# Kernel optimization log

Measured on AMD Instinct MI355X. Metric: run time of the kernel, lower is better.

The kernel has to match this reference:

```python
import jax, jax.numpy as jnp
import numpy as np

B = 65536
IN_DIM = 512
H0, H1 = 256, 128
HEAD_H = 64
D = 12
K_MAX = 3
EPS = 1e-5
# predecessor indices per disease (topologically ordered DAG)
PRED_LISTS = [[], [0], [0], [1, 2], [0, 3], [2], [4, 5], [1, 6], [3, 7], [6, 8], [5, 9], [8, 10, 9]]


def setup_inputs() -> dict:
    key = jax.random.key(0)
    ks = jax.random.split(key, 16)
    x = jax.random.normal(ks[0], (B, IN_DIM), jnp.float32)
    enc_W0 = jax.random.normal(ks[1], (IN_DIM, H0), jnp.float32) * 0.04
    enc_b0 = jnp.zeros((H0,), jnp.float32)
    bn0_g = jnp.ones((H0,), jnp.float32)
    bn0_b = jnp.zeros((H0,), jnp.float32)
    bn0_m = jax.random.normal(ks[2], (H0,), jnp.float32) * 0.1
    bn0_v = jax.random.uniform(ks[3], (H0,), jnp.float32, 0.5, 1.5)
    enc_W1 = jax.random.normal(ks[4], (H0, H1), jnp.float32) * 0.06
    enc_b1 = jnp.zeros((H1,), jnp.float32)
    bn1_g = jnp.ones((H1,), jnp.float32)
    bn1_b = jnp.zeros((H1,), jnp.float32)
    bn1_m = jax.random.normal(ks[5], (H1,), jnp.float32) * 0.1
    bn1_v = jax.random.uniform(ks[6], (H1,), jnp.float32, 0.5, 1.5)
    w_init = jax.random.normal(ks[7], (D, H1), jnp.float32) * 0.09   # head.layer1 (pass-1 logit)
    b_init = jnp.zeros((D,), jnp.float32)
    Wz = jax.random.normal(ks[8], (D, H1, HEAD_H), jnp.float32) * 0.09   # head first layer, z-columns
    Wp = jax.random.normal(ks[9], (D, K_MAX, HEAD_H), jnp.float32) * 0.09  # head first layer, predecessor columns (padded)
    bh = jnp.zeros((D, HEAD_H), jnp.float32)
    Wo = jax.random.normal(ks[10], (D, HEAD_H), jnp.float32) * 0.12
    bo = jnp.zeros((D,), jnp.float32)
    idx = np.zeros((D, K_MAX), np.int32)
    w = np.zeros((D, K_MAX), np.float32)
    for d, preds in enumerate(PRED_LISTS):
        for j, p in enumerate(preds):
            idx[d, j] = p
            w[d, j] = 0.5  # DAG edge weight; zero entries are padding
    return {"x": x, "enc_W0": enc_W0, "enc_b0": enc_b0, "bn0_g": bn0_g, "bn0_b": bn0_b,
            "bn0_m": bn0_m, "bn0_v": bn0_v, "enc_W1": enc_W1, "enc_b1": enc_b1,
            "bn1_g": bn1_g, "bn1_b": bn1_b, "bn1_m": bn1_m, "bn1_v": bn1_v,
            "w_init": w_init, "b_init": b_init, "Wz": Wz, "Wp": Wp, "bh": bh,
            "Wo": Wo, "bo": bo, "pred_w": jnp.asarray(w), "pred_idx": jnp.asarray(idx)}


def reference(x, enc_W0, enc_b0, bn0_g, bn0_b, bn0_m, bn0_v, enc_W1, enc_b1,
              bn1_g, bn1_b, bn1_m, bn1_v, w_init, b_init, Wz, Wp, bh, Wo, bo,
              pred_w, pred_idx):
    # Shared encoder: Linear -> BatchNorm(eval stats) -> ReLU, twice (dropout identity at eval)
    h = x @ enc_W0 + enc_b0
    h = jax.nn.relu((h - bn0_m) * jax.lax.rsqrt(bn0_v + EPS) * bn0_g + bn0_b)
    z = h @ enc_W1 + enc_b1
    z = jax.nn.relu((z - bn1_m) * jax.lax.rsqrt(bn1_v + EPS) * bn1_g + bn1_b)  # [B, H1]
    # Pass 1: initial per-disease prediction = sigmoid(head.layer1(z))
    p = jax.nn.sigmoid(z @ w_init.T + b_init)  # [B, D]
    # Pass 2: DAG gather of predecessor predictions, edge-weighted; padding slots have weight 0
    aug = p[:, pred_idx] * pred_w  # [B, D, K_MAX]
    # Per-disease head: Linear(H1 + k -> HEAD_H) split into z-part + predecessor-part, ReLU, Linear(HEAD_H -> 1), sigmoid
    hid = jax.nn.relu(jnp.einsum('be,deh->bdh', z, Wz) + jnp.einsum('bdk,dkh->bdh', aug, Wp) + bh)
    out = jax.nn.sigmoid(jnp.einsum('bdh,dh->bd', hid, Wo) + bo)  # [B, D] = torch.cat of final_preds
    return out
```

## Files before the change

kernel.cpp:

```cpp
#include <hip/hip_runtime.h>
#include <stdint.h>

#define B_TOT   65536
#define IN_DIM  512
#define H0      256
#define H1      128
#define HH      64
#define NDIS    12

typedef __bf16 bf16_t;
typedef __bf16 bf16x8 __attribute__((ext_vector_type(8)));
typedef float  f32x4  __attribute__((ext_vector_type(4)));

#define WS_W0T   0u
#define WS_W1T   262144u
#define WS_WZT   327680u
#define WS_WIT   524288u
#define WS_AL0   528384u
#define WS_BE0   529408u
#define WS_AL1   530432u
#define WS_BE1   530944u
#define WS_NEED  531456u

#define L_PS     17408u
#define L_PART   21760u
#define L_TOTAL  33792u

__device__ __forceinline__ void dma16(const void* g, void* l) {
    __builtin_amdgcn_global_load_lds(
        (const __attribute__((address_space(1))) unsigned*)g,
        (__attribute__((address_space(3))) unsigned*)l, 16, 0, 0);
}

__device__ __forceinline__ f32x4 MF(bf16x8 a, bf16x8 b, f32x4 c) {
    return __builtin_amdgcn_mfma_f32_16x16x32_bf16(a, b, c, 0, 0, 0);
}

__device__ __forceinline__ bf16x8 xfrag(const float* xb, int row, int sb, int l15) {
    const f32x4 u = *(const f32x4*)(xb + row * 64 + ((( sb    ) ^ l15) << 2));
    const f32x4 v = *(const f32x4*)(xb + row * 64 + (((sb + 1) ^ l15) << 2));
    bf16x8 a;
    a[0]=(bf16_t)u[0]; a[1]=(bf16_t)u[1]; a[2]=(bf16_t)u[2]; a[3]=(bf16_t)u[3];
    a[4]=(bf16_t)v[0]; a[5]=(bf16_t)v[1]; a[6]=(bf16_t)v[2]; a[7]=(bf16_t)v[3];
    return a;
}

__global__ void prep_kernel(const float* __restrict__ W0, const float* __restrict__ b0,
                            const float* __restrict__ g0, const float* __restrict__ bb0,
                            const float* __restrict__ mm0, const float* __restrict__ vv0,
                            const float* __restrict__ W1, const float* __restrict__ b1,
                            const float* __restrict__ g1, const float* __restrict__ bb1,
                            const float* __restrict__ mm1, const float* __restrict__ vv1,
                            const float* __restrict__ w_init, const float* __restrict__ Wz,
                            char* __restrict__ ws)
{
    bf16_t* W0t = (bf16_t*)(ws + WS_W0T);
    bf16_t* W1t = (bf16_t*)(ws + WS_W1T);
    bf16_t* Wzt = (bf16_t*)(ws + WS_WZT);
    bf16_t* wiT = (bf16_t*)(ws + WS_WIT);
    float* al0 = (float*)(ws + WS_AL0);
    float* be0 = (float*)(ws + WS_BE0);
    float* al1 = (float*)(ws + WS_AL1);
    float* be1 = (float*)(ws + WS_BE1);

    int t = blockIdx.x * 256 + threadIdx.x;

    {
        int c = t >> 9, k = t & 511;
        W0t[t] = (bf16_t)W0[k * H0 + c];
    }
    if (t < H1 * H0) {
        int c = t >> 8, k = t & 255;
        W1t[t] = (bf16_t)W1[k * H1 + c];
    }
    if (t < NDIS * HH * H1) {
        int d = t >> 13, r = t & 8191, h = r >> 7, e = r & 127;
        Wzt[t] = (bf16_t)Wz[d * 8192 + e * 64 + h];
    }
    if (t < 16 * H1) {
        int d = t >> 7, e = t & 127;
        wiT[t] = (d < NDIS) ? (bf16_t)w_init[d * H1 + e] : (bf16_t)0.0f;
    }
    if (t < H0) {
        float a = g0[t] * rsqrtf(vv0[t] + 1e-5f);
        al0[t] = a;
        be0[t] = (b0[t] - mm0[t]) * a + bb0[t];
    }
    if (t < H1) {
        float a = g1[t] * rsqrtf(vv1[t] + 1e-5f);
        al1[t] = a;
        be1[t] = (b1[t] - mm1[t]) * a + bb1[t];
    }
}

__global__ __launch_bounds__(256, 4) void fused_kernel(
    const float* __restrict__ x,
    const bf16_t* __restrict__ W0t, const bf16_t* __restrict__ W1t,
    const float* __restrict__ al0, const float* __restrict__ be0,
    const float* __restrict__ al1, const float* __restrict__ be1,
    const bf16_t* __restrict__ Wzt, const bf16_t* __restrict__ wiT,
    const float* __restrict__ b_init, const float* __restrict__ Wp,
    const float* __restrict__ bh, const float* __restrict__ Wo,
    const float* __restrict__ bo, const float* __restrict__ pred_w,
    const int* __restrict__ pred_idx, float* __restrict__ out)
{
    __shared__ __align__(16) char smem[L_TOTAL];

    const int tid  = threadIdx.x;
    const int lane = tid & 63, wid = tid >> 6;
    const int l15 = lane & 15, lg = lane >> 4;
    const int m0 = blockIdx.x * 64;

    const float* xsrcb[4];
    float* xdstb[4];
    #pragma unroll
    for (int i = 0; i < 4; ++i) {
        int row = wid * 16 + i * 4 + (lane >> 4);
        int gs  = (lane & 15) ^ (row & 15);
        xsrcb[i] = x + (size_t)(m0 + row) * IN_DIM + gs * 4;
        xdstb[i] = (float*)smem + (wid * 16 + i * 4) * 64;
    }
#define DMA_STEP(buf, ks) { _Pragma("unroll") \
    for (int i = 0; i < 4; ++i) dma16(xsrcb[i] + (ks) * 64, xdstb[i] + (buf) * 4096); }

    const bf16_t* w0g = W0t + (size_t)(wid * 64 + l15) * IN_DIM + lg * 8;

    f32x4 acc[4][4] = {};

    DMA_STEP(0, 0);
    __syncthreads();

    #pragma unroll 1
    for (int ks = 0; ks < 8; ++ks) {
        if (ks < 7) DMA_STEP((ks + 1) & 1, ks + 1);
        bf16x8 b0[4], b1[4];
        #pragma unroll
        for (int nr = 0; nr < 4; ++nr) {
            b0[nr] = *(const bf16x8*)(w0g + nr * 16 * IN_DIM + ks * 64);
            b1[nr] = *(const bf16x8*)(w0g + nr * 16 * IN_DIM + ks * 64 + 32);
        }
        const float* xb = (const float*)smem + (ks & 1) * 4096;
        #pragma unroll
        for (int mr = 0; mr < 4; ++mr) {
            bf16x8 a = xfrag(xb, mr * 16 + l15, lg * 2, l15);
            #pragma unroll
            for (int nr = 0; nr < 4; ++nr) acc[mr][nr] = MF(a, b0[nr], acc[mr][nr]);
        }
        #pragma unroll
        for (int mr = 0; mr < 4; ++mr) {
            bf16x8 a = xfrag(xb, mr * 16 + l15, 8 + lg * 2, l15);
            #pragma unroll
            for (int nr = 0; nr < 4; ++nr) acc[mr][nr] = MF(a, b1[nr], acc[mr][nr]);
        }
        __syncthreads();
    }

    {
        bf16_t* hs = (bf16_t*)smem;
        #pragma unroll
        for (int nr = 0; nr < 4; ++nr) {
            int c = wid * 64 + nr * 16 + l15;
            float al = al0[c], be = be0[c];
            #pragma unroll
            for (int mr = 0; mr < 4; ++mr)
                #pragma unroll
                for (int j = 0; j < 4; ++j) {
                    int r = mr * 16 + lg * 4 + j;
                    hs[r * 264 + c] = (bf16_t)fmaxf(acc[mr][nr][j] * al + be, 0.f);
                }
        }
    }
    __syncthreads();

    {
        const bf16_t* hs  = (const bf16_t*)smem;
        const bf16_t* w1g = W1t + (size_t)(wid * 32 + l15) * H0 + lg * 8;
        f32x4 acc2[4][2] = {};
        #pragma unroll 1
        for (int kf = 0; kf < 8; ++kf) {
            bf16x8 bw0 = *(const bf16x8*)(w1g + kf * 32);
            bf16x8 bw1 = *(const bf16x8*)(w1g + 16 * H0 + kf * 32);
            #pragma unroll
            for (int mr = 0; mr < 4; ++mr) {
                bf16x8 a = *(const bf16x8*)(hs + (mr * 16 + l15) * 264 + kf * 32 + lg * 8);
                acc2[mr][0] = MF(a, bw0, acc2[mr][0]);
                acc2[mr][1] = MF(a, bw1, acc2[mr][1]);
            }
        }
        __syncthreads();
        bf16_t* zs = (bf16_t*)smem;
        #pragma unroll
        for (int nr = 0; nr < 2; ++nr) {
            int c = wid * 32 + nr * 16 + l15;
            float al = al1[c], be = be1[c];
            #pragma unroll
            for (int mr = 0; mr < 4; ++mr)
                #pragma unroll
                for (int j = 0; j < 4; ++j) {
                    int r = mr * 16 + lg * 4 + j;
                    zs[r * 136 + c] = (bf16_t)fmaxf(acc2[mr][nr][j] * al + be, 0.f);
                }
        }
    }
    __syncthreads();

    const bf16_t* zs = (const bf16_t*)smem;
    float* psf  = (float*)(smem + L_PS);
    float* part = (float*)(smem + L_PART);
    const bf16_t* wzg = Wzt + (size_t)(wid * 16 + l15) * H1 + lg * 8;

    bf16x8 az0 = *(const bf16x8*)(wzg);
    bf16x8 az1 = *(const bf16x8*)(wzg + 32);
    bf16x8 az2 = *(const bf16x8*)(wzg + 64);
    bf16x8 az3 = *(const bf16x8*)(wzg + 96);

    {
        f32x4 pacc = {};
        #pragma unroll
        for (int kf = 0; kf < 4; ++kf) {
            bf16x8 aw = *(const bf16x8*)(wiT + l15 * H1 + kf * 32 + lg * 8);
            bf16x8 bz = *(const bf16x8*)(zs + (wid * 16 + l15) * 136 + kf * 32 + lg * 8);
            pacc = MF(aw, bz, pacc);
        }
        #pragma unroll
        for (int j = 0; j < 4; ++j) {
            int d = lg * 4 + j;
            float bi = (d < NDIS) ? b_init[d] : 0.f;
            psf[(wid * 16 + l15) * 17 + d] = 1.f / (1.f + __expf(-(pacc[j] + bi)));
        }
    }
    __syncthreads();

    #pragma unroll 1
    for (int d = 0; d < NDIS; ++d) {
        bf16x8 an0 = az0, an1 = az1, an2 = az2, an3 = az3;
        if (d < NDIS - 1) {
            const bf16_t* p = wzg + (size_t)(d + 1) * 8192;
            an0 = *(const bf16x8*)(p);
            an1 = *(const bf16x8*)(p + 32);
            an2 = *(const bf16x8*)(p + 64);
            an3 = *(const bf16x8*)(p + 96);
        }
        f32x4 hacc[4] = {};
        #pragma unroll
        for (int nr = 0; nr < 4; ++nr) {
            const bf16_t* zr = zs + (nr * 16 + l15) * 136 + lg * 8;
            hacc[nr] = MF(az0, *(const bf16x8*)(zr),      hacc[nr]);
            hacc[nr] = MF(az1, *(const bf16x8*)(zr + 32), hacc[nr]);
            hacc[nr] = MF(az2, *(const bf16x8*)(zr + 64), hacc[nr]);
            hacc[nr] = MF(az3, *(const bf16x8*)(zr + 96), hacc[nr]);
        }
        int i0 = pred_idx[d * 3 + 0], i1 = pred_idx[d * 3 + 1], i2 = pred_idx[d * 3 + 2];
        float wq0 = pred_w[d * 3 + 0], wq1 = pred_w[d * 3 + 1], wq2 = pred_w[d * 3 + 2];
        float bhv[4], wov[4], wpa[4], wpb[4], wpc[4];
        #pragma unroll
        for (int j = 0; j < 4; ++j) {
            int h = wid * 16 + lg * 4 + j;
            bhv[j] = bh[d * 64 + h];
            wov[j] = Wo[d * 64 + h];
            wpa[j] = Wp[d * 192 + h];
            wpb[j] = Wp[d * 192 + 64 + h];
            wpc[j] = Wp[d * 192 + 128 + h];
        }
        #pragma unroll
        for (int nr = 0; nr < 4; ++nr) {
            int r = nr * 16 + l15;
            float a0 = psf[r * 17 + i0] * wq0;
            float a1 = psf[r * 17 + i1] * wq1;
            float a2 = psf[r * 17 + i2] * wq2;
            float s = 0.f;
            #pragma unroll
            for (int j = 0; j < 4; ++j) {
                float v = hacc[nr][j] + bhv[j] + a0 * wpa[j] + a1 * wpb[j] + a2 * wpc[j];
                s += fmaxf(v, 0.f) * wov[j];
            }
            s += __shfl_xor(s, 16);
            s += __shfl_xor(s, 32);
            if (lane < 16) part[(d & 1) * 256 + r * 4 + wid] = s;
        }
        __syncthreads();
        if (tid < 64) {
            f32x4 p4 = *(const f32x4*)(part + (d & 1) * 256 + tid * 4);
            float s = p4[0] + p4[1] + p4[2] + p4[3] + bo[d];
            out[(size_t)(m0 + tid) * NDIS + d] = 1.f / (1.f + __expf(-s));
        }
        az0 = an0; az1 = an1; az2 = an2; az3 = an3;
    }
}

extern "C" void kernel_launch(void* const* d_in, const int* in_sizes, int n_in,
                              void* d_out, int out_size, void* d_ws, size_t ws_size,
                              hipStream_t stream) {
    if (ws_size < (size_t)WS_NEED) return;

    const float* x      = (const float*)d_in[0];
    const float* W0     = (const float*)d_in[1];
    const float* b0     = (const float*)d_in[2];
    const float* g0     = (const float*)d_in[3];
    const float* bb0    = (const float*)d_in[4];
    const float* mm0    = (const float*)d_in[5];
    const float* vv0    = (const float*)d_in[6];
    const float* W1     = (const float*)d_in[7];
    const float* b1     = (const float*)d_in[8];
    const float* g1     = (const float*)d_in[9];
    const float* bb1    = (const float*)d_in[10];
    const float* mm1    = (const float*)d_in[11];
    const float* vv1    = (const float*)d_in[12];
    const float* w_init = (const float*)d_in[13];
    const float* b_init = (const float*)d_in[14];
    const float* Wz     = (const float*)d_in[15];
    const float* Wp     = (const float*)d_in[16];
    const float* bh     = (const float*)d_in[17];
    const float* Wo     = (const float*)d_in[18];
    const float* bo     = (const float*)d_in[19];
    const float* pred_w = (const float*)d_in[20];
    const int*   pred_idx = (const int*)d_in[21];

    char* ws = (char*)d_ws;
    const bf16_t* W0t = (const bf16_t*)(ws + WS_W0T);
    const bf16_t* W1t = (const bf16_t*)(ws + WS_W1T);
    const bf16_t* Wzt = (const bf16_t*)(ws + WS_WZT);
    const bf16_t* wiT = (const bf16_t*)(ws + WS_WIT);
    const float* al0 = (const float*)(ws + WS_AL0);
    const float* be0 = (const float*)(ws + WS_BE0);
    const float* al1 = (const float*)(ws + WS_AL1);
    const float* be1 = (const float*)(ws + WS_BE1);

    prep_kernel<<<dim3(512), dim3(256), 0, stream>>>(
        W0, b0, g0, bb0, mm0, vv0, W1, b1, g1, bb1, mm1, vv1, w_init, Wz, ws);

    fused_kernel<<<dim3(B_TOT / 64), dim3(256), 0, stream>>>(
        x, W0t, W1t, al0, be0, al1, be1, Wzt, wiT, b_init, Wp, bh, Wo, bo,
        pred_w, pred_idx, (float*)d_out);
}
```

Measured before the change: 95.06 us.

## Stage x as bf16 in LDS via registers and drop per-disease barriers

Replaces the direct global-to-LDS fp32 DMA of x with register-prefetched loads. Each value is converted to bf16 once and stored swizzled, which halves the LDS tile and removes the repeated per-fragment conversion. It also swaps the MFMA operand roles for the encoder GEMMs, unrolls GEMM2 with double-buffered weight prefetch, and vectorizes the BN epilogue stores and parameter loads. The 12 per-disease barriers go away: all partial sums are kept in LDS and the output is written once as a coalesced block. In exchange it uses more LDS, raises register pressure from the prefetch buffers, and relies on a custom waitcnt+barrier.

```diff
diff --git a/kernel.cpp b/kernel.cpp
--- a/kernel.cpp
+++ b/kernel.cpp
@@ -9,6 +9,7 @@
 #define NDIS    12
 
 typedef __bf16 bf16_t;
+typedef __bf16 bf16x4 __attribute__((ext_vector_type(4)));
 typedef __bf16 bf16x8 __attribute__((ext_vector_type(8)));
 typedef float  f32x4  __attribute__((ext_vector_type(4)));
 
@@ -23,27 +24,18 @@
 #define WS_NEED  531456u
 
 #define L_PS     17408u
-#define L_PART   21760u
-#define L_TOTAL  33792u
-
-__device__ __forceinline__ void dma16(const void* g, void* l) {
-    __builtin_amdgcn_global_load_lds(
-        (const __attribute__((address_space(1))) unsigned*)g,
-        (__attribute__((address_space(3))) unsigned*)l, 16, 0, 0);
-}
+#define L_PART   22528u
+#define L_TOTAL  34816u
 
 __device__ __forceinline__ f32x4 MF(bf16x8 a, bf16x8 b, f32x4 c) {
     return __builtin_amdgcn_mfma_f32_16x16x32_bf16(a, b, c, 0, 0, 0);
 }
-
-__device__ __forceinline__ bf16x8 xfrag(const float* xb, int row, int sb, int l15) {
-    const f32x4 u = *(const f32x4*)(xb + row * 64 + ((( sb    ) ^ l15) << 2));
-    const f32x4 v = *(const f32x4*)(xb + row * 64 + (((sb + 1) ^ l15) << 2));
-    bf16x8 a;
-    a[0]=(bf16_t)u[0]; a[1]=(bf16_t)u[1]; a[2]=(bf16_t)u[2]; a[3]=(bf16_t)u[3];
-    a[4]=(bf16_t)v[0]; a[5]=(bf16_t)v[1]; a[6]=(bf16_t)v[2]; a[7]=(bf16_t)v[3];
-    return a;
-}
+__device__ __forceinline__ void BAR() {
+    asm volatile("s_waitcnt lgkmcnt(0)\n\ts_barrier" ::: "memory");
+}
+
+#define PACK8(o, lo, hi) { o[0]=(bf16_t)lo[0]; o[1]=(bf16_t)lo[1]; o[2]=(bf16_t)lo[2]; o[3]=(bf16_t)lo[3]; \
+                           o[4]=(bf16_t)hi[0]; o[5]=(bf16_t)hi[1]; o[6]=(bf16_t)hi[2]; o[7]=(bf16_t)hi[3]; }
 
 __global__ void prep_kernel(const float* __restrict__ W0, const float* __restrict__ b0,
                             const float* __restrict__ g0, const float* __restrict__ bb0,
@@ -111,98 +103,137 @@
     const int l15 = lane & 15, lg = lane >> 4;
     const int m0 = blockIdx.x * 64;
 
-    const float* xsrcb[4];
-    float* xdstb[4];
-    #pragma unroll
-    for (int i = 0; i < 4; ++i) {
-        int row = wid * 16 + i * 4 + (lane >> 4);
-        int gs  = (lane & 15) ^ (row & 15);
-        xsrcb[i] = x + (size_t)(m0 + row) * IN_DIM + gs * 4;
-        xdstb[i] = (float*)smem + (wid * 16 + i * 4) * 64;
-    }
-#define DMA_STEP(buf, ks) { _Pragma("unroll") \
-    for (int i = 0; i < 4; ++i) dma16(xsrcb[i] + (ks) * 64, xdstb[i] + (buf) * 4096); }
-
-    const bf16_t* w0g = W0t + (size_t)(wid * 64 + l15) * IN_DIM + lg * 8;
+    bf16_t* xs = (bf16_t*)smem;
+
+    const float *sgp0, *sgp1;
+    int sd0, sd1;
+    {
+        int f0 = tid, f1 = tid + 256;
+        int r0 = f0 >> 3, s0 = f0 & 7, r1 = f1 >> 3, s1 = f1 & 7;
+        sgp0 = x + (size_t)(m0 + r0) * IN_DIM + s0 * 8;
+        sgp1 = x + (size_t)(m0 + r1) * IN_DIM + s1 * 8;
+        sd0 = r0 * 64 + ((s0 ^ (r0 & 7)) << 3);
+        sd1 = r1 * 64 + ((s1 ^ (r1 & 7)) << 3);
+    }
+    const bf16_t* wg = W0t + (size_t)(wid * 64 + l15) * IN_DIM + lg * 8;
+    const int xb0 = ((lg ^ (l15 & 7)) << 3);
+    const int xb1 = (((4 | lg) ^ (l15 & 7)) << 3);
+    const int xrow = l15 * 64;
 
     f32x4 acc[4][4] = {};
-
-    DMA_STEP(0, 0);
-    __syncthreads();
+    f32x4 lo0, hi0, lo1, hi1;
+
+    lo0 = *(const f32x4*)(sgp0);     hi0 = *(const f32x4*)(sgp0 + 4);
+    lo1 = *(const f32x4*)(sgp1);     hi1 = *(const f32x4*)(sgp1 + 4);
+    { bf16x8 o; PACK8(o, lo0, hi0); *(bf16x8*)(xs + sd0) = o; }
+    { bf16x8 o; PACK8(o, lo1, hi1); *(bf16x8*)(xs + sd1) = o; }
+    lo0 = *(const f32x4*)(sgp0 + 64); hi0 = *(const f32x4*)(sgp0 + 68);
+    lo1 = *(const f32x4*)(sgp1 + 64); hi1 = *(const f32x4*)(sgp1 + 68);
+    BAR();
 
     #pragma unroll 1
     for (int ks = 0; ks < 8; ++ks) {
-        if (ks < 7) DMA_STEP((ks + 1) & 1, ks + 1);
-        bf16x8 b0[4], b1[4];
-        #pragma unroll
-        for (int nr = 0; nr < 4; ++nr) {
-            b0[nr] = *(const bf16x8*)(w0g + nr * 16 * IN_DIM + ks * 64);
-            b1[nr] = *(const bf16x8*)(w0g + nr * 16 * IN_DIM + ks * 64 + 32);
-        }
-        const float* xb = (const float*)smem + (ks & 1) * 4096;
-        #pragma unroll
-        for (int mr = 0; mr < 4; ++mr) {
-            bf16x8 a = xfrag(xb, mr * 16 + l15, lg * 2, l15);
-            #pragma unroll
-            for (int nr = 0; nr < 4; ++nr) acc[mr][nr] = MF(a, b0[nr], acc[mr][nr]);
-        }
-        #pragma unroll
-        for (int mr = 0; mr < 4; ++mr) {
-            bf16x8 a = xfrag(xb, mr * 16 + l15, 8 + lg * 2, l15);
-            #pragma unroll
-            for (int nr = 0; nr < 4; ++nr) acc[mr][nr] = MF(a, b1[nr], acc[mr][nr]);
-        }
-        __syncthreads();
+        bf16x8 a0[4], a1[4];
+        #pragma unroll
+        for (int mf = 0; mf < 4; ++mf) {
+            a0[mf] = *(const bf16x8*)(wg + mf * 16 * IN_DIM + ks * 64);
+            a1[mf] = *(const bf16x8*)(wg + mf * 16 * IN_DIM + ks * 64 + 32);
+        }
+        if (ks < 7) {
+            bf16_t* xw = xs + ((ks + 1) & 1) * 4096;
+            { bf16x8 o; PACK8(o, lo0, hi0); *(bf16x8*)(xw + sd0) = o; }
+            { bf16x8 o; PACK8(o, lo1, hi1); *(bf16x8*)(xw + sd1) = o; }
+            if (ks < 6) {
+                lo0 = *(const f32x4*)(sgp0 + (ks + 2) * 64); hi0 = *(const f32x4*)(sgp0 + (ks + 2) * 64 + 4);
+                lo1 = *(const f32x4*)(sgp1 + (ks + 2) * 64); hi1 = *(const f32x4*)(sgp1 + (ks + 2) * 64 + 4);
+            }
+        }
+        const bf16_t* xr = xs + (ks & 1) * 4096;
+        #pragma unroll
+        for (int nf = 0; nf < 4; ++nf) {
+            bf16x8 b = *(const bf16x8*)(xr + nf * 1024 + xrow + xb0);
+            #pragma unroll
+            for (int mf = 0; mf < 4; ++mf) acc[mf][nf] = MF(a0[mf], b, acc[mf][nf]);
+        }
+        #pragma unroll
+        for (int nf = 0; nf < 4; ++nf) {
+            bf16x8 b = *(const bf16x8*)(xr + nf * 1024 + xrow + xb1);
+            #pragma unroll
+            for (int mf = 0; mf < 4; ++mf) acc[mf][nf] = MF(a1[mf], b, acc[mf][nf]);
+        }
+        BAR();
     }
 
     {
         bf16_t* hs = (bf16_t*)smem;
         #pragma unroll
-        for (int nr = 0; nr < 4; ++nr) {
-            int c = wid * 64 + nr * 16 + l15;
-            float al = al0[c], be = be0[c];
-            #pragma unroll
-            for (int mr = 0; mr < 4; ++mr)
+        for (int mf = 0; mf < 4; ++mf) {
+            int c = wid * 64 + mf * 16 + lg * 4;
+            f32x4 al = *(const f32x4*)(al0 + c);
+            f32x4 be = *(const f32x4*)(be0 + c);
+            #pragma unroll
+            for (int nf = 0; nf < 4; ++nf) {
+                int r = nf * 16 + l15;
+                bf16x4 o;
                 #pragma unroll
-                for (int j = 0; j < 4; ++j) {
-                    int r = mr * 16 + lg * 4 + j;
-                    hs[r * 264 + c] = (bf16_t)fmaxf(acc[mr][nr][j] * al + be, 0.f);
-                }
-        }
-    }
-    __syncthreads();
-
+                for (int j = 0; j < 4; ++j)
+                    o[j] = (bf16_t)fmaxf(acc[mf][nf][j] * al[j] + be[j], 0.f);
+                *(bf16x4*)(hs + r * 264 + c) = o;
+            }
+        }
+    }
+    BAR();
+
+    f32x4 acc2[2][4] = {};
     {
         const bf16_t* hs  = (const bf16_t*)smem;
         const bf16_t* w1g = W1t + (size_t)(wid * 32 + l15) * H0 + lg * 8;
-        f32x4 acc2[4][2] = {};
-        #pragma unroll 1
+        bf16x8 aP[2], aQ[2];
+        aP[0] = *(const bf16x8*)(w1g);
+        aP[1] = *(const bf16x8*)(w1g + 16 * H0);
+        aQ[0] = *(const bf16x8*)(w1g + 32);
+        aQ[1] = *(const bf16x8*)(w1g + 16 * H0 + 32);
+        #pragma unroll
         for (int kf = 0; kf < 8; ++kf) {
-            bf16x8 bw0 = *(const bf16x8*)(w1g + kf * 32);
-            bf16x8 bw1 = *(const bf16x8*)(w1g + 16 * H0 + kf * 32);
-            #pragma unroll
-            for (int mr = 0; mr < 4; ++mr) {
-                bf16x8 a = *(const bf16x8*)(hs + (mr * 16 + l15) * 264 + kf * 32 + lg * 8);
-                acc2[mr][0] = MF(a, bw0, acc2[mr][0]);
-                acc2[mr][1] = MF(a, bw1, acc2[mr][1]);
-            }
-        }
-        __syncthreads();
+            bf16x8 ac0 = (kf & 1) ? aQ[0] : aP[0];
+            bf16x8 ac1 = (kf & 1) ? aQ[1] : aP[1];
+            if (kf < 6) {
+                if (kf & 1) {
+                    aQ[0] = *(const bf16x8*)(w1g + (kf + 2) * 32);
+                    aQ[1] = *(const bf16x8*)(w1g + 16 * H0 + (kf + 2) * 32);
+                } else {
+                    aP[0] = *(const bf16x8*)(w1g + (kf + 2) * 32);
+                    aP[1] = *(const bf16x8*)(w1g + 16 * H0 + (kf + 2) * 32);
+                }
+            }
+            #pragma unroll
+            for (int nf = 0; nf < 4; ++nf) {
+                bf16x8 b = *(const bf16x8*)(hs + (nf * 16 + l15) * 264 + kf * 32 + lg * 8);
+                acc2[0][nf] = MF(ac0, b, acc2[0][nf]);
+                acc2[1][nf] = MF(ac1, b, acc2[1][nf]);
+            }
+        }
+    }
+    BAR();
+    {
         bf16_t* zs = (bf16_t*)smem;
         #pragma unroll
-        for (int nr = 0; nr < 2; ++nr) {
-            int c = wid * 32 + nr * 16 + l15;
-            float al = al1[c], be = be1[c];
-            #pragma unroll
-            for (int mr = 0; mr < 4; ++mr)
+        for (int mf = 0; mf < 2; ++mf) {
+            int c = wid * 32 + mf * 16 + lg * 4;
+            f32x4 al = *(const f32x4*)(al1 + c);
+            f32x4 be = *(const f32x4*)(be1 + c);
+            #pragma unroll
+            for (int nf = 0; nf < 4; ++nf) {
+                int r = nf * 16 + l15;
+                bf16x4 o;
                 #pragma unroll
-                for (int j = 0; j < 4; ++j) {
-                    int r = mr * 16 + lg * 4 + j;
-                    zs[r * 136 + c] = (bf16_t)fmaxf(acc2[mr][nr][j] * al + be, 0.f);
-                }
-        }
-    }
-    __syncthreads();
+                for (int j = 0; j < 4; ++j)
+                    o[j] = (bf16_t)fmaxf(acc2[mf][nf][j] * al[j] + be[j], 0.f);
+                *(bf16x4*)(zs + r * 136 + c) = o;
+            }
+        }
+    }
+    BAR();
 
     const bf16_t* zs = (const bf16_t*)smem;
     float* psf  = (float*)(smem + L_PS);
@@ -222,69 +253,75 @@
             bf16x8 bz = *(const bf16x8*)(zs + (wid * 16 + l15) * 136 + kf * 32 + lg * 8);
             pacc = MF(aw, bz, pacc);
         }
+        f32x4 pv;
         #pragma unroll
         for (int j = 0; j < 4; ++j) {
             int d = lg * 4 + j;
             float bi = (d < NDIS) ? b_init[d] : 0.f;
-            psf[(wid * 16 + l15) * 17 + d] = 1.f / (1.f + __expf(-(pacc[j] + bi)));
-        }
-    }
-    __syncthreads();
+            pv[j] = 1.f / (1.f + __expf(-(pacc[j] + bi)));
+        }
+        *(f32x4*)(psf + (wid * 16 + l15) * 20 + lg * 4) = pv;
+    }
+    BAR();
 
     #pragma unroll 1
     for (int d = 0; d < NDIS; ++d) {
         bf16x8 an0 = az0, an1 = az1, an2 = az2, an3 = az3;
         if (d < NDIS - 1) {
             const bf16_t* p = wzg + (size_t)(d + 1) * 8192;
-            an0 = *(const bf16x8*)(p);
-            an1 = *(const bf16x8*)(p + 32);
-            an2 = *(const bf16x8*)(p + 64);
-            an3 = *(const bf16x8*)(p + 96);
-        }
-        f32x4 hacc[4] = {};
-        #pragma unroll
-        for (int nr = 0; nr < 4; ++nr) {
-            const bf16_t* zr = zs + (nr * 16 + l15) * 136 + lg * 8;
-            hacc[nr] = MF(az0, *(const bf16x8*)(zr),      hacc[nr]);
-            hacc[nr] = MF(az1, *(const bf16x8*)(zr + 32), hacc[nr]);
-            hacc[nr] = MF(az2, *(const bf16x8*)(zr + 64), hacc[nr]);
-            hacc[nr] = MF(az3, *(const bf16x8*)(zr + 96), hacc[nr]);
+            an0 = *(const bf16x8*)(p);      an1 = *(const bf16x8*)(p + 32);
+            an2 = *(const bf16x8*)(p + 64); an3 = *(const bf16x8*)(p + 96);
         }
         int i0 = pred_idx[d * 3 + 0], i1 = pred_idx[d * 3 + 1], i2 = pred_idx[d * 3 + 2];
         float wq0 = pred_w[d * 3 + 0], wq1 = pred_w[d * 3 + 1], wq2 = pred_w[d * 3 + 2];
-        float bhv[4], wov[4], wpa[4], wpb[4], wpc[4];
-        #pragma unroll
-        for (int j = 0; j < 4; ++j) {
-            int h = wid * 16 + lg * 4 + j;
-            bhv[j] = bh[d * 64 + h];
-            wov[j] = Wo[d * 64 + h];
-            wpa[j] = Wp[d * 192 + h];
-            wpb[j] = Wp[d * 192 + 64 + h];
-            wpc[j] = Wp[d * 192 + 128 + h];
-        }
-        #pragma unroll
-        for (int nr = 0; nr < 4; ++nr) {
-            int r = nr * 16 + l15;
-            float a0 = psf[r * 17 + i0] * wq0;
-            float a1 = psf[r * 17 + i1] * wq1;
-            float a2 = psf[r * 17 + i2] * wq2;
+        int hb = wid * 16 + lg * 4;
+        f32x4 bhv = *(const f32x4*)(bh + d * 64 + hb);
+        f32x4 wov = *(const f32x4*)(Wo + d * 64 + hb);
+        f32x4 wpa = *(const f32x4*)(Wp + d * 192 + hb);
+        f32x4 wpb = *(const f32x4*)(Wp + d * 192 + 64 + hb);
+        f32x4 wpc = *(const f32x4*)(Wp + d * 192 + 128 + hb);
+
+        #pragma unroll
+        for (int nf = 0; nf < 4; ++nf) {
+            const bf16_t* zr = zs + (nf * 16 + l15) * 136 + lg * 8;
+            f32x4 hacc = {};
+            hacc = MF(az0, *(const bf16x8*)(zr),      hacc);
+            hacc = MF(az1, *(const bf16x8*)(zr + 32), hacc);
+            hacc = MF(az2, *(const bf16x8*)(zr + 64), hacc);
+            hacc = MF(az3, *(const bf16x8*)(zr + 96), hacc);
+            int r = nf * 16 + l15;
+            float a0 = psf[r * 20 + i0] * wq0;
+            float a1 = psf[r * 20 + i1] * wq1;
+            float a2 = psf[r * 20 + i2] * wq2;
             float s = 0.f;
             #pragma unroll
             for (int j = 0; j < 4; ++j) {
-                float v = hacc[nr][j] + bhv[j] + a0 * wpa[j] + a1 * wpb[j] + a2 * wpc[j];
+                float v = hacc[j] + bhv[j] + a0 * wpa[j] + a1 * wpb[j] + a2 * wpc[j];
                 s += fmaxf(v, 0.f) * wov[j];
             }
             s += __shfl_xor(s, 16);
             s += __shfl_xor(s, 32);
-            if (lane < 16) part[(d & 1) * 256 + r * 4 + wid] = s;
-        }
-        __syncthreads();
-        if (tid < 64) {
-            f32x4 p4 = *(const f32x4*)(part + (d & 1) * 256 + tid * 4);
-            float s = p4[0] + p4[1] + p4[2] + p4[3] + bo[d];
-            out[(size_t)(m0 + tid) * NDIS + d] = 1.f / (1.f + __expf(-s));
+            if (lane < 16) part[d * 256 + r * 4 + wid] = s;
         }
         az0 = an0; az1 = an1; az2 = an2; az3 = an3;
+    }
+    BAR();
+
+    {
+        float* obuf = (float*)(smem + L_PS);
+        #pragma unroll
+        for (int i = 0; i < 3; ++i) {
+            int e = tid * 3 + i;
+            int d = e % 12, r = e / 12;
+            f32x4 p = *(const f32x4*)(part + d * 256 + r * 4);
+            float s = p[0] + p[1] + p[2] + p[3] + bo[d];
+            obuf[e] = 1.f / (1.f + __expf(-s));
+        }
+    }
+    BAR();
+    if (tid < 192) {
+        f32x4 o = *(const f32x4*)((const float*)(smem + L_PS) + tid * 4);
+        *(f32x4*)(out + (size_t)blockIdx.x * 768 + tid * 4) = o;
     }
 }
 
```

Result: no change. 94.30 us (-0.8%).
